# Optimization experiments

Hardware: AMD Instinct MI355X
Metric: run time of the kernel (lower is better)

The kernel has to match this reference:

```python
import jax, jax.numpy as jnp
import numpy as np

N = 50000  # num nodes
D = 128    # feature / hidden size
E = 500000 # edges per edge type


def _mean_agg(h, src, dst):
    # gather src features, segment-mean onto dst; zero-in-degree nodes -> 0 (DGL semantics)
    nsum = jax.ops.segment_sum(h[src], dst, num_segments=N)  # [N, D]
    deg = jax.ops.segment_sum(jnp.ones((src.shape[0],), h.dtype), dst, num_segments=N)
    return nsum / jnp.maximum(deg, 1.0)[:, None]


def _sage_layer(h, src, dst, w_self, w_neigh, b):
    # DGL SAGEConv, aggregator_type='mean'
    hn = _mean_agg(h, src, dst)
    return h @ w_self + hn @ w_neigh + b


def _hetero_layer(h, src0, dst0, src1, dst1, w_self, w_neigh, b):
    # HeteroGraphConv(aggregate='sum') with the SAME SAGEConv shared across both edge types
    return (_sage_layer(h, src0, dst0, w_self, w_neigh, b)
            + _sage_layer(h, src1, dst1, w_self, w_neigh, b))


def setup_inputs() -> dict:
    key = jax.random.key(0)
    ks = jax.random.split(key, 11)
    s = 1.0 / np.sqrt(D)
    return {
        "h": jax.random.normal(ks[0], (N, D), dtype=jnp.float32),
        "src0": jax.random.randint(ks[1], (E,), 0, N),
        "dst0": jax.random.randint(ks[2], (E,), 0, N),
        "src1": jax.random.randint(ks[3], (E,), 0, N),
        "dst1": jax.random.randint(ks[4], (E,), 0, N),
        "w_self1": jax.random.uniform(ks[5], (D, D), jnp.float32, -s, s),
        "w_neigh1": jax.random.uniform(ks[6], (D, D), jnp.float32, -s, s),
        "b1": jnp.zeros((D,), jnp.float32),
        "w_self2": jax.random.uniform(ks[7], (D, D), jnp.float32, -s, s),
        "w_neigh2": jax.random.uniform(ks[8], (D, D), jnp.float32, -s, s),
        "b2": jnp.zeros((D,), jnp.float32),
    }


def reference(h, src0, dst0, src1, dst1,
              w_self1, w_neigh1, b1, w_self2, w_neigh2, b2):
    # layer 1 + ReLU (ReLU applied to all but last layer)
    h = _hetero_layer(h, src0, dst0, src1, dst1, w_self1, w_neigh1, b1)
    h = jax.nn.relu(h)
    # layer 2 (no ReLU)
    h = _hetero_layer(h, src0, dst0, src1, dst1, w_self2, w_neigh2, b2)
    return h
```

## Files before the change

### kernel.cpp

```cpp
#include <hip/hip_runtime.h>

#define NN 50000
#define DD 128
#define EE 500000

typedef __attribute__((ext_vector_type(8))) unsigned short ushort8;
typedef __attribute__((ext_vector_type(8))) short bf16x8v;
typedef __attribute__((ext_vector_type(4))) float f32x4;

static __device__ __forceinline__ unsigned short f2bf(float f) {
    unsigned int u = __float_as_uint(f);
    unsigned int r = (u + 0x7fffu + ((u >> 16) & 1u)) >> 16;
    return (unsigned short)r;
}
static __device__ __forceinline__ float bf2f(unsigned short s) {
    return __uint_as_float(((unsigned int)s) << 16);
}

__global__ __launch_bounds__(256) void cvt_kernel(const float* __restrict__ h,
                                                  unsigned short* __restrict__ A1) {
    size_t i = ((size_t)blockIdx.x * 256 + threadIdx.x) * 8;
    int m = (int)(i >> 7);
    int d = (int)(i & 127);
    float4 a = *reinterpret_cast<const float4*>(&h[i]);
    float4 b = *reinterpret_cast<const float4*>(&h[i + 4]);
    ushort8 o;
    o[0] = f2bf(2.f * a.x); o[1] = f2bf(2.f * a.y); o[2] = f2bf(2.f * a.z); o[3] = f2bf(2.f * a.w);
    o[4] = f2bf(2.f * b.x); o[5] = f2bf(2.f * b.y); o[6] = f2bf(2.f * b.z); o[7] = f2bf(2.f * b.w);
    *reinterpret_cast<ushort8*>(&A1[(size_t)m * 256 + d]) = o;
}

__global__ __launch_bounds__(256) void wprep_kernel(const float* __restrict__ Ws1,
                                                    const float* __restrict__ Wn1,
                                                    const float* __restrict__ Ws2,
                                                    const float* __restrict__ Wn2,
                                                    unsigned short* __restrict__ Bt1,
                                                    unsigned short* __restrict__ Bt2) {
    int t = blockIdx.x * 256 + threadIdx.x;
    int lay = t >> 15;
    int r = t & 32767;
    int k = r >> 7;
    int n = r & 127;
    const float* Ws = lay ? Ws2 : Ws1;
    const float* Wn = lay ? Wn2 : Wn1;
    unsigned short* Bt = lay ? Bt2 : Bt1;
    float v = (k < 128) ? Ws[(size_t)k * 128 + n] : Wn[(size_t)(k - 128) * 128 + n];
    Bt[(size_t)n * 256 + k] = f2bf(v);
}

__global__ __launch_bounds__(256) void degi_kernel(const int* __restrict__ dst0,
                                                   const int* __restrict__ dst1,
                                                   int* __restrict__ deg0,
                                                   int* __restrict__ deg1) {
    int i = blockIdx.x * 256 + threadIdx.x;
    if (i < EE) {
        atomicAdd(&deg0[dst0[i]], 1);
        atomicAdd(&deg1[dst1[i]], 1);
    }
}

__global__ __launch_bounds__(1024) void scan_kernel(const int* __restrict__ deg0,
                                                    const int* __restrict__ deg1,
                                                    int* __restrict__ rp0,
                                                    int* __restrict__ rp1) {
    const int* deg = blockIdx.x ? deg1 : deg0;
    int* rp = blockIdx.x ? rp1 : rp0;
    __shared__ int spart[1024];
    int running = 0;
    for (int base = 0; base < NN; base += 8192) {
        int i0 = base + threadIdx.x * 8;
        int v[8];
        int local = 0;
#pragma unroll
        for (int j = 0; j < 8; ++j) {
            int idx = i0 + j;
            v[j] = (idx < NN) ? deg[idx] : 0;
            local += v[j];
        }
        spart[threadIdx.x] = local;
        __syncthreads();
        for (int off = 1; off < 1024; off <<= 1) {
            int t = (threadIdx.x >= off) ? spart[threadIdx.x - off] : 0;
            __syncthreads();
            spart[threadIdx.x] += t;
            __syncthreads();
        }
        int excl = running + spart[threadIdx.x] - local;
        int total = spart[1023];
#pragma unroll
        for (int j = 0; j < 8; ++j) {
            int idx = i0 + j;
            if (idx < NN) rp[idx] = excl;
            excl += v[j];
        }
        running += total;
        __syncthreads();
    }
    if (threadIdx.x == 0) rp[NN] = running;
}

__global__ __launch_bounds__(256) void rdegi_kernel(const int* __restrict__ deg0,
                                                    const int* __restrict__ deg1,
                                                    float* __restrict__ rdeg0,
                                                    float* __restrict__ rdeg1) {
    int i = blockIdx.x * 256 + threadIdx.x;
    if (i < NN) {
        rdeg0[i] = 1.0f / fmaxf((float)deg0[i], 1.0f);
        rdeg1[i] = 1.0f / fmaxf((float)deg1[i], 1.0f);
    }
}

__global__ __launch_bounds__(256) void fill_kernel(const int* __restrict__ src0,
                                                   const int* __restrict__ dst0,
                                                   const int* __restrict__ src1,
                                                   const int* __restrict__ dst1,
                                                   const int* __restrict__ rp0,
                                                   int* __restrict__ cur0,
                                                   int* __restrict__ csr0,
                                                   const int* __restrict__ rp1,
                                                   int* __restrict__ cur1,
                                                   int* __restrict__ csr1) {
    int e = blockIdx.x * 256 + threadIdx.x;
    if (e < EE) {
        int d0 = dst0[e];
        int p0 = atomicAdd(&cur0[d0], 1);
        csr0[rp0[d0] + p0] = src0[e];
        int d1 = dst1[e];
        int p1 = atomicAdd(&cur1[d1], 1);
        csr1[rp1[d1] + p1] = src1[e];
    }
}

__global__ __launch_bounds__(256) void agg_gather_kernel(unsigned short* __restrict__ A,
                                                         const int* __restrict__ rp0,
                                                         const int* __restrict__ csr0,
                                                         const int* __restrict__ rp1,
                                                         const int* __restrict__ csr1,
                                                         const float* __restrict__ rdeg0,
                                                         const float* __restrict__ rdeg1) {
    int tid  = threadIdx.x;
    int node = blockIdx.x * 4 + (tid >> 6);
    int lane = tid & 63;
    int sub  = lane >> 4;
    int lc   = lane & 15;

    float a0[8] = {0.f, 0.f, 0.f, 0.f, 0.f, 0.f, 0.f, 0.f};
    float a1[8] = {0.f, 0.f, 0.f, 0.f, 0.f, 0.f, 0.f, 0.f};

    int b0 = rp0[node], e0 = rp0[node + 1];
    for (int e = b0 + sub; e < e0; e += 4) {
        int s = csr0[e];
        ushort8 v = *reinterpret_cast<const ushort8*>(&A[(size_t)s * 256 + lc * 8]);
#pragma unroll
        for (int j = 0; j < 8; ++j) a0[j] += bf2f(v[j]);
    }
    int b1 = rp1[node], e1 = rp1[node + 1];
    for (int e = b1 + sub; e < e1; e += 4) {
        int s = csr1[e];
        ushort8 v = *reinterpret_cast<const ushort8*>(&A[(size_t)s * 256 + lc * 8]);
#pragma unroll
        for (int j = 0; j < 8; ++j) a1[j] += bf2f(v[j]);
    }

    float r0 = 0.5f * rdeg0[node], r1 = 0.5f * rdeg1[node];
    float g[8];
#pragma unroll
    for (int j = 0; j < 8; ++j) {
        g[j] = a0[j] * r0 + a1[j] * r1;
        g[j] += __shfl_xor(g[j], 16);
        g[j] += __shfl_xor(g[j], 32);
    }
    if (sub == 0) {
        ushort8 o;
#pragma unroll
        for (int j = 0; j < 8; ++j) o[j] = f2bf(g[j]);
        *reinterpret_cast<ushort8*>(&A[(size_t)node * 256 + 128 + lc * 8]) = o;
    }
}

__global__ __launch_bounds__(256) void mfma_gemm_kernel(const unsigned short* __restrict__ A,
                                                        const unsigned short* __restrict__ Bt,
                                                        const float* __restrict__ bias,
                                                        float* __restrict__ outf,
                                                        unsigned short* __restrict__ a2self,
                                                        int relu) {
    const int tid  = threadIdx.x;
    const int wave = tid >> 6;
    const int lane = tid & 63;
    const int lr   = lane & 15;
    const int lk   = (lane >> 4) * 8;
    const int rowbase = blockIdx.x * 64 + wave * 16;

    int arow = rowbase + lr;
    if (arow >= NN) arow = NN - 1;
    const unsigned short* Ap = A + (size_t)arow * 256 + lk;
    const unsigned short* Bp = Bt + (size_t)lr * 256 + lk;

    f32x4 acc[8];
#pragma unroll
    for (int cf = 0; cf < 8; ++cf) acc[cf] = (f32x4){0.f, 0.f, 0.f, 0.f};

    for (int ks = 0; ks < 8; ++ks) {
        bf16x8v a = *reinterpret_cast<const bf16x8v*>(Ap + ks * 32);
#pragma unroll
        for (int cf = 0; cf < 8; ++cf) {
            bf16x8v b = *reinterpret_cast<const bf16x8v*>(Bp + cf * (16 * 256) + ks * 32);
            acc[cf] = __builtin_amdgcn_mfma_f32_16x16x32_bf16(a, b, acc[cf], 0, 0, 0);
        }
    }

    const int rfrag = (lane >> 4) * 4;
#pragma unroll
    for (int cf = 0; cf < 8; ++cf) {
        int col = cf * 16 + lr;
        float bb = 2.0f * bias[col];
#pragma unroll
        for (int rg = 0; rg < 4; ++rg) {
            int r = rowbase + rfrag + rg;
            if (r < NN) {
                float v = acc[cf][rg] + bb;
                if (relu) v = fmaxf(v, 0.f);
                if (outf) {
                    outf[(size_t)r * 128 + col] = v;
                } else {
                    a2self[(size_t)r * 256 + col] = f2bf(2.0f * v);
                }
            }
        }
    }
}

extern "C" void kernel_launch(void* const* d_in, const int* in_sizes, int n_in,
                              void* d_out, int out_size, void* d_ws, size_t ws_size,
                              hipStream_t stream) {
    (void)in_sizes; (void)n_in; (void)out_size; (void)ws_size;

    const float* h    = (const float*)d_in[0];
    const int*   src0 = (const int*)d_in[1];
    const int*   dst0 = (const int*)d_in[2];
    const int*   src1 = (const int*)d_in[3];
    const int*   dst1 = (const int*)d_in[4];
    const float* Ws1  = (const float*)d_in[5];
    const float* Wn1  = (const float*)d_in[6];
    const float* b1   = (const float*)d_in[7];
    const float* Ws2  = (const float*)d_in[8];
    const float* Wn2  = (const float*)d_in[9];
    const float* b2   = (const float*)d_in[10];
    float* out = (float*)d_out;

    const size_t ND  = (size_t)NN * DD;
    const size_t ND2 = (size_t)NN * 256;

    unsigned short* A1  = (unsigned short*)d_ws;
    unsigned short* A2  = A1 + ND2;
    unsigned short* Bt1 = A2 + ND2;
    unsigned short* Bt2 = Bt1 + 32768;
    float* rdeg0 = (float*)(Bt2 + 32768);
    float* rdeg1 = rdeg0 + NN;
    int* deg0 = (int*)(rdeg1 + NN);
    int* deg1 = deg0 + NN;
    int* cur0 = deg1 + NN;
    int* cur1 = cur0 + NN;
    int* rp0  = cur1 + NN;
    int* rp1  = rp0 + NN + 1;
    int* csr0 = rp1 + NN + 1;
    int* csr1 = csr0 + EE;

    const int eBlocks    = (EE + 255) / 256;
    const int nBlocks    = (NN + 255) / 256;
    const int cvtBlocks  = (int)(ND / (256 * 8));
    const int aggBlocks  = NN / 4;
    const int gemmBlocks = (NN + 63) / 64;

    hipMemsetAsync(deg0, 0, 4 * (size_t)NN * sizeof(int), stream);
    cvt_kernel<<<cvtBlocks, 256, 0, stream>>>(h, A1);
    wprep_kernel<<<256, 256, 0, stream>>>(Ws1, Wn1, Ws2, Wn2, Bt1, Bt2);
    degi_kernel<<<eBlocks, 256, 0, stream>>>(dst0, dst1, deg0, deg1);
    scan_kernel<<<2, 1024, 0, stream>>>(deg0, deg1, rp0, rp1);
    rdegi_kernel<<<nBlocks, 256, 0, stream>>>(deg0, deg1, rdeg0, rdeg1);
    fill_kernel<<<eBlocks, 256, 0, stream>>>(src0, dst0, src1, dst1,
                                             rp0, cur0, csr0, rp1, cur1, csr1);

    agg_gather_kernel<<<aggBlocks, 256, 0, stream>>>(A1, rp0, csr0, rp1, csr1, rdeg0, rdeg1);
    mfma_gemm_kernel<<<gemmBlocks, 256, 0, stream>>>(A1, Bt1, b1, nullptr, A2, 1);

    agg_gather_kernel<<<aggBlocks, 256, 0, stream>>>(A2, rp0, csr0, rp1, csr1, rdeg0, rdeg1);
    mfma_gemm_kernel<<<gemmBlocks, 256, 0, stream>>>(A2, Bt2, b2, out, nullptr, 0);
}
```

Before: 377.7 us.

## Fuse prep kernels and replace single-block scan with multi-block three-pass scan

Merges the h-to-bf16 conversion, the weight transpose and the degree counting into one launch, cutting launch count. The two-block 1024-thread serial scan is replaced by a parallel three-pass scan over 196 blocks per edge type. The last pass also writes rdeg and initialises the fill cursors to the row starts, so fill no longer reads rp and the memset shrinks. It adds two more small launches for the scan, and the CSR neighbour order still depends on atomic ordering as before.

```diff
diff --git a/kernel.cpp b/kernel.cpp
--- a/kernel.cpp
+++ b/kernel.cpp
@@ -3,6 +3,11 @@
 #define NN 50000
 #define DD 128
 #define EE 500000
+
+#define PREP_CVT 3125
+#define PREP_W   256
+#define PREP_E   1954
+#define SCAN_B   196
 
 typedef __attribute__((ext_vector_type(8))) unsigned short ushort8;
 typedef __attribute__((ext_vector_type(8))) short bf16x8v;
@@ -17,96 +22,121 @@
     return __uint_as_float(((unsigned int)s) << 16);
 }
 
-__global__ __launch_bounds__(256) void cvt_kernel(const float* __restrict__ h,
-                                                  unsigned short* __restrict__ A1) {
-    size_t i = ((size_t)blockIdx.x * 256 + threadIdx.x) * 8;
-    int m = (int)(i >> 7);
-    int d = (int)(i & 127);
-    float4 a = *reinterpret_cast<const float4*>(&h[i]);
-    float4 b = *reinterpret_cast<const float4*>(&h[i + 4]);
-    ushort8 o;
-    o[0] = f2bf(2.f * a.x); o[1] = f2bf(2.f * a.y); o[2] = f2bf(2.f * a.z); o[3] = f2bf(2.f * a.w);
-    o[4] = f2bf(2.f * b.x); o[5] = f2bf(2.f * b.y); o[6] = f2bf(2.f * b.z); o[7] = f2bf(2.f * b.w);
-    *reinterpret_cast<ushort8*>(&A1[(size_t)m * 256 + d]) = o;
-}
-
-__global__ __launch_bounds__(256) void wprep_kernel(const float* __restrict__ Ws1,
-                                                    const float* __restrict__ Wn1,
-                                                    const float* __restrict__ Ws2,
-                                                    const float* __restrict__ Wn2,
-                                                    unsigned short* __restrict__ Bt1,
-                                                    unsigned short* __restrict__ Bt2) {
-    int t = blockIdx.x * 256 + threadIdx.x;
-    int lay = t >> 15;
-    int r = t & 32767;
-    int k = r >> 7;
-    int n = r & 127;
-    const float* Ws = lay ? Ws2 : Ws1;
-    const float* Wn = lay ? Wn2 : Wn1;
-    unsigned short* Bt = lay ? Bt2 : Bt1;
-    float v = (k < 128) ? Ws[(size_t)k * 128 + n] : Wn[(size_t)(k - 128) * 128 + n];
-    Bt[(size_t)n * 256 + k] = f2bf(v);
-}
-
-__global__ __launch_bounds__(256) void degi_kernel(const int* __restrict__ dst0,
+__global__ __launch_bounds__(256) void prep_kernel(const float* __restrict__ h,
+                                                   unsigned short* __restrict__ A1,
+                                                   const float* __restrict__ Ws1,
+                                                   const float* __restrict__ Wn1,
+                                                   const float* __restrict__ Ws2,
+                                                   const float* __restrict__ Wn2,
+                                                   unsigned short* __restrict__ Bt1,
+                                                   unsigned short* __restrict__ Bt2,
+                                                   const int* __restrict__ dst0,
                                                    const int* __restrict__ dst1,
                                                    int* __restrict__ deg0,
                                                    int* __restrict__ deg1) {
-    int i = blockIdx.x * 256 + threadIdx.x;
-    if (i < EE) {
-        atomicAdd(&deg0[dst0[i]], 1);
-        atomicAdd(&deg1[dst1[i]], 1);
-    }
-}
-
-__global__ __launch_bounds__(1024) void scan_kernel(const int* __restrict__ deg0,
+    int blk = blockIdx.x;
+    if (blk < PREP_CVT) {
+        size_t i = ((size_t)blk * 256 + threadIdx.x) * 8;
+        int m = (int)(i >> 7);
+        int d = (int)(i & 127);
+        float4 a = *reinterpret_cast<const float4*>(&h[i]);
+        float4 b = *reinterpret_cast<const float4*>(&h[i + 4]);
+        ushort8 o;
+        o[0] = f2bf(2.f * a.x); o[1] = f2bf(2.f * a.y); o[2] = f2bf(2.f * a.z); o[3] = f2bf(2.f * a.w);
+        o[4] = f2bf(2.f * b.x); o[5] = f2bf(2.f * b.y); o[6] = f2bf(2.f * b.z); o[7] = f2bf(2.f * b.w);
+        *reinterpret_cast<ushort8*>(&A1[(size_t)m * 256 + d]) = o;
+    } else if (blk < PREP_CVT + PREP_W) {
+        int t = (blk - PREP_CVT) * 256 + threadIdx.x;
+        int lay = t >> 15;
+        int r = t & 32767;
+        int k = r >> 7;
+        int n = r & 127;
+        const float* Ws = lay ? Ws2 : Ws1;
+        const float* Wn = lay ? Wn2 : Wn1;
+        unsigned short* Bt = lay ? Bt2 : Bt1;
+        float v = (k < 128) ? Ws[(size_t)k * 128 + n] : Wn[(size_t)(k - 128) * 128 + n];
+        Bt[(size_t)n * 256 + k] = f2bf(v);
+    } else {
+        int e = (blk - PREP_CVT - PREP_W) * 256 + threadIdx.x;
+        if (e < EE) {
+            atomicAdd(&deg0[dst0[e]], 1);
+            atomicAdd(&deg1[dst1[e]], 1);
+        }
+    }
+}
+
+__global__ __launch_bounds__(256) void scan1_kernel(const int* __restrict__ deg0,
                                                     const int* __restrict__ deg1,
-                                                    int* __restrict__ rp0,
-                                                    int* __restrict__ rp1) {
-    const int* deg = blockIdx.x ? deg1 : deg0;
-    int* rp = blockIdx.x ? rp1 : rp0;
-    __shared__ int spart[1024];
-    int running = 0;
-    for (int base = 0; base < NN; base += 8192) {
-        int i0 = base + threadIdx.x * 8;
-        int v[8];
-        int local = 0;
-#pragma unroll
-        for (int j = 0; j < 8; ++j) {
-            int idx = i0 + j;
-            v[j] = (idx < NN) ? deg[idx] : 0;
-            local += v[j];
-        }
-        spart[threadIdx.x] = local;
-        __syncthreads();
-        for (int off = 1; off < 1024; off <<= 1) {
-            int t = (threadIdx.x >= off) ? spart[threadIdx.x - off] : 0;
+                                                    int* __restrict__ part) {
+    int b = blockIdx.x;
+    int type = (b >= SCAN_B);
+    int bb = b - type * SCAN_B;
+    const int* deg = type ? deg1 : deg0;
+    int i = bb * 256 + threadIdx.x;
+    int v = (i < NN) ? deg[i] : 0;
+    __shared__ int s[256];
+    s[threadIdx.x] = v;
+    __syncthreads();
+    for (int off = 1; off < 256; off <<= 1) {
+        int t = (threadIdx.x >= off) ? s[threadIdx.x - off] : 0;
+        __syncthreads();
+        s[threadIdx.x] += t;
+        __syncthreads();
+    }
+    if (threadIdx.x == 255) part[b] = s[255];
+}
+
+__global__ __launch_bounds__(256) void scan2_kernel(int* __restrict__ part) {
+    __shared__ int s[256];
+    for (int type = 0; type < 2; ++type) {
+        int idx = type * SCAN_B + threadIdx.x;
+        int v = (threadIdx.x < SCAN_B) ? part[idx] : 0;
+        s[threadIdx.x] = v;
+        __syncthreads();
+        for (int off = 1; off < 256; off <<= 1) {
+            int t = (threadIdx.x >= off) ? s[threadIdx.x - off] : 0;
             __syncthreads();
-            spart[threadIdx.x] += t;
+            s[threadIdx.x] += t;
             __syncthreads();
         }
-        int excl = running + spart[threadIdx.x] - local;
-        int total = spart[1023];
-#pragma unroll
-        for (int j = 0; j < 8; ++j) {
-            int idx = i0 + j;
-            if (idx < NN) rp[idx] = excl;
-            excl += v[j];
-        }
-        running += total;
-        __syncthreads();
-    }
-    if (threadIdx.x == 0) rp[NN] = running;
-}
-
-__global__ __launch_bounds__(256) void rdegi_kernel(const int* __restrict__ deg0,
+        if (threadIdx.x < SCAN_B) part[idx] = s[threadIdx.x] - v;
+        __syncthreads();
+    }
+}
+
+__global__ __launch_bounds__(256) void scan3_kernel(const int* __restrict__ deg0,
                                                     const int* __restrict__ deg1,
+                                                    const int* __restrict__ part,
+                                                    int* __restrict__ rp0,
+                                                    int* __restrict__ rp1,
+                                                    int* __restrict__ cur0,
+                                                    int* __restrict__ cur1,
                                                     float* __restrict__ rdeg0,
                                                     float* __restrict__ rdeg1) {
-    int i = blockIdx.x * 256 + threadIdx.x;
+    int b = blockIdx.x;
+    int type = (b >= SCAN_B);
+    int bb = b - type * SCAN_B;
+    const int* deg = type ? deg1 : deg0;
+    int* rp  = type ? rp1 : rp0;
+    int* cur = type ? cur1 : cur0;
+    float* rdeg = type ? rdeg1 : rdeg0;
+    int i = bb * 256 + threadIdx.x;
+    int v = (i < NN) ? deg[i] : 0;
+    __shared__ int s[256];
+    s[threadIdx.x] = v;
+    __syncthreads();
+    for (int off = 1; off < 256; off <<= 1) {
+        int t = (threadIdx.x >= off) ? s[threadIdx.x - off] : 0;
+        __syncthreads();
+        s[threadIdx.x] += t;
+        __syncthreads();
+    }
+    int excl = s[threadIdx.x] - v + part[b];
     if (i < NN) {
-        rdeg0[i] = 1.0f / fmaxf((float)deg0[i], 1.0f);
-        rdeg1[i] = 1.0f / fmaxf((float)deg1[i], 1.0f);
+        rp[i] = excl;
+        cur[i] = excl;
+        rdeg[i] = 1.0f / fmaxf((float)v, 1.0f);
+        if (i == NN - 1) rp[NN] = excl + v;
     }
 }
 
@@ -114,20 +144,16 @@
                                                    const int* __restrict__ dst0,
                                                    const int* __restrict__ src1,
                                                    const int* __restrict__ dst1,
-                                                   const int* __restrict__ rp0,
                                                    int* __restrict__ cur0,
                                                    int* __restrict__ csr0,
-                                                   const int* __restrict__ rp1,
                                                    int* __restrict__ cur1,
                                                    int* __restrict__ csr1) {
     int e = blockIdx.x * 256 + threadIdx.x;
     if (e < EE) {
-        int d0 = dst0[e];
-        int p0 = atomicAdd(&cur0[d0], 1);
-        csr0[rp0[d0] + p0] = src0[e];
-        int d1 = dst1[e];
-        int p1 = atomicAdd(&cur1[d1], 1);
-        csr1[rp1[d1] + p1] = src1[e];
+        int p0 = atomicAdd(&cur0[dst0[e]], 1);
+        csr0[p0] = src0[e];
+        int p1 = atomicAdd(&cur1[dst1[e]], 1);
+        csr1[p1] = src1[e];
     }
 }
 
@@ -248,7 +274,6 @@
     const float* b2   = (const float*)d_in[10];
     float* out = (float*)d_out;
 
-    const size_t ND  = (size_t)NN * DD;
     const size_t ND2 = (size_t)NN * 256;
 
     unsigned short* A1  = (unsigned short*)d_ws;
@@ -263,23 +288,23 @@
     int* cur1 = cur0 + NN;
     int* rp0  = cur1 + NN;
     int* rp1  = rp0 + NN + 1;
-    int* csr0 = rp1 + NN + 1;
+    int* part = rp1 + NN + 1;
+    int* csr0 = part + 2 * SCAN_B;
     int* csr1 = csr0 + EE;
 
-    const int eBlocks    = (EE + 255) / 256;
-    const int nBlocks    = (NN + 255) / 256;
-    const int cvtBlocks  = (int)(ND / (256 * 8));
+    const int prepBlocks = PREP_CVT + PREP_W + PREP_E;
     const int aggBlocks  = NN / 4;
     const int gemmBlocks = (NN + 63) / 64;
 
-    hipMemsetAsync(deg0, 0, 4 * (size_t)NN * sizeof(int), stream);
-    cvt_kernel<<<cvtBlocks, 256, 0, stream>>>(h, A1);
-    wprep_kernel<<<256, 256, 0, stream>>>(Ws1, Wn1, Ws2, Wn2, Bt1, Bt2);
-    degi_kernel<<<eBlocks, 256, 0, stream>>>(dst0, dst1, deg0, deg1);
-    scan_kernel<<<2, 1024, 0, stream>>>(deg0, deg1, rp0, rp1);
-    rdegi_kernel<<<nBlocks, 256, 0, stream>>>(deg0, deg1, rdeg0, rdeg1);
-    fill_kernel<<<eBlocks, 256, 0, stream>>>(src0, dst0, src1, dst1,
-                                             rp0, cur0, csr0, rp1, cur1, csr1);
+    hipMemsetAsync(deg0, 0, 2 * (size_t)NN * sizeof(int), stream);
+    prep_kernel<<<prepBlocks, 256, 0, stream>>>(h, A1, Ws1, Wn1, Ws2, Wn2, Bt1, Bt2,
+                                                dst0, dst1, deg0, deg1);
+    scan1_kernel<<<2 * SCAN_B, 256, 0, stream>>>(deg0, deg1, part);
+    scan2_kernel<<<1, 256, 0, stream>>>(part);
+    scan3_kernel<<<2 * SCAN_B, 256, 0, stream>>>(deg0, deg1, part,
+                                                 rp0, rp1, cur0, cur1, rdeg0, rdeg1);
+    fill_kernel<<<PREP_E, 256, 0, stream>>>(src0, dst0, src1, dst1,
+                                            cur0, csr0, cur1, csr1);
 
     agg_gather_kernel<<<aggBlocks, 256, 0, stream>>>(A1, rp0, csr0, rp1, csr1, rdeg0, rdeg1);
     mfma_gemm_kernel<<<gemmBlocks, 256, 0, stream>>>(A1, Bt1, b1, nullptr, A2, 1);
```

After: 378.9 us. About the same (+0.3%).
